# Kernel tuning notes

Hardware: AMD Instinct MI355X
Metric: run time of the kernel (lower is better)

## Reference

```python
import jax, jax.numpy as jnp
import numpy as np

N_NODES = 100000


def _gin_layer(x, edge_index, Wa, ba, Wb, bb):
    # GINConv, eps=0: h_i = MLP(x_i + sum_{j->i} x_j)
    src, dst = edge_index[0], edge_index[1]
    agg = jax.ops.segment_sum(x[src], dst, num_segments=N_NODES)  # [N, d]
    h = x + agg
    h = jax.nn.relu(h @ Wa + ba) @ Wb + bb
    return h


def setup_inputs() -> dict:
    key = jax.random.key(0)
    ks = jax.random.split(key, 8)
    d_in, d_h, E = 128, 128, 1600000
    scale_in = 1.0 / np.sqrt(d_in)
    scale_h = 1.0 / np.sqrt(d_h)
    return {
        "x": jax.random.normal(ks[0], (N_NODES, d_in), dtype=jnp.float32),
        "edge_index": jax.random.randint(ks[1], (2, E), 0, N_NODES, dtype=jnp.int64),
        "batch": jnp.zeros((N_NODES,), dtype=jnp.int64),
        "W1a": jax.random.normal(ks[2], (d_in, d_h), dtype=jnp.float32) * scale_in,
        "b1a": jnp.zeros((d_h,), dtype=jnp.float32),
        "W1b": jax.random.normal(ks[3], (d_h, d_h), dtype=jnp.float32) * scale_h,
        "b1b": jnp.zeros((d_h,), dtype=jnp.float32),
        "W2a": jax.random.normal(ks[4], (d_h, d_h), dtype=jnp.float32) * scale_h,
        "b2a": jnp.zeros((d_h,), dtype=jnp.float32),
        "W2b": jax.random.normal(ks[5], (d_h, d_h), dtype=jnp.float32) * scale_h,
        "b2b": jnp.zeros((d_h,), dtype=jnp.float32),
    }


def reference(x, edge_index, batch, W1a, b1a, W1b, b1b, W2a, b2a, W2b, b2b):
    h = jax.nn.relu(_gin_layer(x, edge_index, W1a, b1a, W1b, b1b))
    h = jax.nn.relu(_gin_layer(h, edge_index, W2a, b2a, W2b, b2b))
    return h
```

## Files before the change

kernel.cpp:

```cpp
#include <hip/hip_runtime.h>
#include <hip/hip_bf16.h>

#define D 128
#define EPB 4096
#define CAP 6144

typedef float f32x4 __attribute__((ext_vector_type(4)));
typedef short short8 __attribute__((ext_vector_type(8)));


__device__ __forceinline__ unsigned bf16_rtn_bits(float x) {
    unsigned u = __float_as_uint(x);
    return (u + 0x7fffu + ((u >> 16) & 1u)) >> 16;
}

__device__ __forceinline__ void addbf8(float* acc, uint4 v) {
    acc[0] += __uint_as_float(v.x << 16);
    acc[1] += __uint_as_float(v.x & 0xffff0000u);
    acc[2] += __uint_as_float(v.y << 16);
    acc[3] += __uint_as_float(v.y & 0xffff0000u);
    acc[4] += __uint_as_float(v.z << 16);
    acc[5] += __uint_as_float(v.z & 0xffff0000u);
    acc[6] += __uint_as_float(v.w << 16);
    acc[7] += __uint_as_float(v.w & 0xffff0000u);
}


__global__ void k_zero(int* __restrict__ p, int n) {
    int i = blockIdx.x * 256 + threadIdx.x;
    if (i < n) p[i] = 0;
}

__global__ __launch_bounds__(256) void k_xtobf(const float4* __restrict__ X, uint4* __restrict__ O, int n8) {
    int i = blockIdx.x * 256 + threadIdx.x;
    if (i >= n8) return;
    float4 a = X[2 * i], b = X[2 * i + 1];
    uint4 o;
    o.x = bf16_rtn_bits(a.x) | (bf16_rtn_bits(a.y) << 16);
    o.y = bf16_rtn_bits(a.z) | (bf16_rtn_bits(a.w) << 16);
    o.z = bf16_rtn_bits(b.x) | (bf16_rtn_bits(b.y) << 16);
    o.w = bf16_rtn_bits(b.z) | (bf16_rtn_bits(b.w) << 16);
    O[i] = o;
}

__global__ void k_wsplit(const float* __restrict__ W, unsigned short* __restrict__ Wt) {
    int i = blockIdx.x * 256 + threadIdx.x;
    int k = i >> 7, n = i & 127;
    Wt[n * 128 + k] = (unsigned short)bf16_rtn_bits(W[i]);
}


__global__ __launch_bounds__(256) void k_bin(const int* __restrict__ src,
                                             const int* __restrict__ dst, int E,
                                             int* __restrict__ gCursor,
                                             unsigned* __restrict__ binned) {
    __shared__ int cnt[512];
    __shared__ int offs[512];
    __shared__ int c2[512];
    __shared__ int gOff[512];
    __shared__ int s[256];
    __shared__ unsigned staged[EPB];
    __shared__ unsigned short bo[EPB];
    int t = threadIdx.x;
    cnt[t] = 0; cnt[t + 256] = 0;
    c2[t] = 0; c2[t + 256] = 0;
    __syncthreads();

    unsigned pk[EPB / 256];
    int bk[EPB / 256];
    int e0 = blockIdx.x * EPB;
#pragma unroll
    for (int i = 0; i < EPB / 256; ++i) {
        int e = e0 + i * 256 + t;
        int b = -1; unsigned p = 0;
        if (e < E) {
            int dv = dst[e], sv = src[e];
            b = dv >> 8;
            p = ((unsigned)sv << 8) | (unsigned)(dv & 255);
            atomicAdd(&cnt[b], 1);
        }
        pk[i] = p; bk[i] = b;
    }
    __syncthreads();
    int v0 = cnt[2 * t], v1 = cnt[2 * t + 1];
    int ps = v0 + v1;
    s[t] = ps;
    __syncthreads();
    for (int off = 1; off < 256; off <<= 1) {
        int tv = (t >= off) ? s[t - off] : 0;
        __syncthreads();
        s[t] += tv;
        __syncthreads();
    }
    int ex = s[t] - ps;
    offs[2 * t] = ex;
    offs[2 * t + 1] = ex + v0;
    if (cnt[2 * t])     gOff[2 * t]     = atomicAdd(&gCursor[2 * t], cnt[2 * t]);
    if (cnt[2 * t + 1]) gOff[2 * t + 1] = atomicAdd(&gCursor[2 * t + 1], cnt[2 * t + 1]);
    __syncthreads();
#pragma unroll
    for (int i = 0; i < EPB / 256; ++i) {
        int b = bk[i];
        if (b >= 0) {
            int p = offs[b] + atomicAdd(&c2[b], 1);
            staged[p] = pk[i];
            bo[p] = (unsigned short)b;
        }
    }
    __syncthreads();
    int total = s[255];
    for (int p = t; p < total; p += 256) {
        int b = bo[p];
        binned[(size_t)b * CAP + gOff[b] + (p - offs[b])] = staged[p];
    }
}

__global__ __launch_bounds__(256) void k_csr(const unsigned* __restrict__ binned,
                                             const int* __restrict__ bucketCnt,
                                             int* __restrict__ alloc,
                                             int2* __restrict__ rowse,
                                             int* __restrict__ colA,
                                             int Nn) {
    __shared__ int hist[256], loc[256], cur[256], s[256];
    __shared__ int baseSh;
    int t = threadIdx.x, b = blockIdx.x;
    int n = bucketCnt[b];
    const unsigned* bp = binned + (size_t)b * CAP;
    hist[t] = 0; cur[t] = 0;
    __syncthreads();
    for (int i = t; i < n; i += 256) atomicAdd(&hist[bp[i] & 255u], 1);
    __syncthreads();
    int v = hist[t];
    s[t] = v;
    __syncthreads();
    for (int off = 1; off < 256; off <<= 1) {
        int tv = (t >= off) ? s[t - off] : 0;
        __syncthreads();
        s[t] += tv;
        __syncthreads();
    }
    loc[t] = s[t] - v;
    if (t == 255) baseSh = atomicAdd(alloc, s[255]);
    __syncthreads();
    int base = baseSh;
    int node = b * 256 + t;
    if (node < Nn) rowse[node] = make_int2(base + loc[t], base + loc[t] + v);
    for (int i = t; i < n; i += 256) {
        unsigned w = bp[i];
        int dl = (int)(w & 255u);
        int p = atomicAdd(&cur[dl], 1);
        colA[base + loc[dl] + p] = (int)(w >> 8);
    }
}


__global__ __launch_bounds__(256) void agg_bf16(const unsigned short* __restrict__ X,
                                                const int2* __restrict__ rowse,
                                                const int* __restrict__ colA,
                                                unsigned short* __restrict__ H, int nnodes) {
    int node = blockIdx.x * 4 + (threadIdx.x >> 6);
    if (node >= nnodes) return;
    int lane = threadIdx.x & 63;
    int qt = lane >> 4, slot = lane & 15;
    const uint4* x4 = (const uint4*)X;
    size_t base = (size_t)node * 16 + slot;

    int2 se = rowse[node];
    int e = se.x, end = se.y;

    float acc[8] = {0.f, 0.f, 0.f, 0.f, 0.f, 0.f, 0.f, 0.f};
    float acc2[8] = {0.f, 0.f, 0.f, 0.f, 0.f, 0.f, 0.f, 0.f};
    if (qt == 0) addbf8(acc, x4[base]);

    for (; e + 16 <= end; e += 16) {
        int s0 = colA[e + qt];
        int s1 = colA[e + 4 + qt];
        int s2 = colA[e + 8 + qt];
        int s3 = colA[e + 12 + qt];
        uint4 v0 = x4[(size_t)s0 * 16 + slot];
        uint4 v1 = x4[(size_t)s1 * 16 + slot];
        uint4 v2 = x4[(size_t)s2 * 16 + slot];
        uint4 v3 = x4[(size_t)s3 * 16 + slot];
        addbf8(acc, v0);
        addbf8(acc2, v1);
        addbf8(acc, v2);
        addbf8(acc2, v3);
    }
    if (e + 8 <= end) {
        int s0 = colA[e + qt];
        int s1 = colA[e + 4 + qt];
        uint4 v0 = x4[(size_t)s0 * 16 + slot];
        uint4 v1 = x4[(size_t)s1 * 16 + slot];
        addbf8(acc, v0);
        addbf8(acc2, v1);
        e += 8;
    }
    for (; e < end; e += 4) {
        int idx = e + qt;
        if (idx < end) {
            int s = colA[idx];
            addbf8(acc, x4[(size_t)s * 16 + slot]);
        }
    }
#pragma unroll
    for (int j = 0; j < 8; ++j) {
        acc[j] += acc2[j];
        acc[j] += __shfl_xor(acc[j], 16);
        acc[j] += __shfl_xor(acc[j], 32);
    }
    if (qt == 0) {
        uint4 o;
        o.x = bf16_rtn_bits(acc[0]) | (bf16_rtn_bits(acc[1]) << 16);
        o.y = bf16_rtn_bits(acc[2]) | (bf16_rtn_bits(acc[3]) << 16);
        o.z = bf16_rtn_bits(acc[4]) | (bf16_rtn_bits(acc[5]) << 16);
        o.w = bf16_rtn_bits(acc[6]) | (bf16_rtn_bits(acc[7]) << 16);
        ((uint4*)H)[base] = o;
    }
}


template <bool OUT_BF16>
__global__ __launch_bounds__(256) void mlp_mfma(const unsigned short* __restrict__ Hb,
                                                const unsigned short* __restrict__ WaT,
                                                const float* __restrict__ ba,
                                                const unsigned short* __restrict__ WbT,
                                                const float* __restrict__ bb,
                                                void* __restrict__ OutP, int nrows) {
    __shared__ unsigned short sh[64 * 128];
    const int tid = threadIdx.x;
    const int rows0 = blockIdx.x * 64;
    const int nvalid = min(64, nrows - rows0);

    const int wv = tid >> 6, l = tid & 63, q = l >> 4, cl = l & 15;

    short8 B1[2][4], B2[2][4];
#pragma unroll
    for (int cf = 0; cf < 2; ++cf) {
        const unsigned short* wa = WaT + (size_t)(wv * 32 + cf * 16 + cl) * 128 + q * 8;
        const unsigned short* wb = WbT + (size_t)(wv * 32 + cf * 16 + cl) * 128 + q * 8;
#pragma unroll
        for (int kk = 0; kk < 4; ++kk) {
            B1[cf][kk] = *(const short8*)(wa + kk * 32);
            B2[cf][kk] = *(const short8*)(wb + kk * 32);
        }
    }

    {
        const uint4* src = (const uint4*)(Hb + (size_t)rows0 * 128);
#pragma unroll
        for (int it = 0; it < 4; ++it) {
            int idx = it * 256 + tid;
            int row = idx >> 4, s16 = idx & 15;
            uint4 v = {0u, 0u, 0u, 0u};
            if (row < nvalid) v = src[idx];
            int byteoff = (row << 8) + ((s16 << 4) ^ ((row & 7) << 4));
            *(uint4*)((char*)sh + byteoff) = v;
        }
    }
    __syncthreads();

    f32x4 acc[4][2];
#pragma unroll
    for (int cf = 0; cf < 2; ++cf) {
        float bv = ba[wv * 32 + cf * 16 + cl];
        f32x4 a = {bv, bv, bv, bv};
#pragma unroll
        for (int m = 0; m < 4; ++m) acc[m][cf] = a;
    }
#pragma unroll
    for (int kk = 0; kk < 4; ++kk) {
        short8 a[4];
#pragma unroll
        for (int m = 0; m < 4; ++m) {
            int row = m * 16 + cl;
            int byteoff = (row << 8) + ((kk * 64 + q * 16) ^ ((row & 7) << 4));
            a[m] = *(const short8*)((const char*)sh + byteoff);
        }
#pragma unroll
        for (int m = 0; m < 4; ++m)
#pragma unroll
            for (int cf = 0; cf < 2; ++cf)
                acc[m][cf] = __builtin_amdgcn_mfma_f32_16x16x32_bf16(a[m], B1[cf][kk], acc[m][cf], 0, 0, 0);
    }
    __syncthreads();

#pragma unroll
    for (int m = 0; m < 4; ++m)
#pragma unroll
        for (int cf = 0; cf < 2; ++cf)
#pragma unroll
            for (int r = 0; r < 4; ++r) {
                int row = m * 16 + q * 4 + r;
                int col = wv * 32 + cf * 16 + cl;
                int byteoff = (row << 8) + ((col * 2) ^ ((row & 7) << 4));
                *(unsigned short*)((char*)sh + byteoff) =
                    (unsigned short)bf16_rtn_bits(fmaxf(acc[m][cf][r], 0.f));
            }
    __syncthreads();

#pragma unroll
    for (int cf = 0; cf < 2; ++cf) {
        float bv = bb[wv * 32 + cf * 16 + cl];
        f32x4 a = {bv, bv, bv, bv};
#pragma unroll
        for (int m = 0; m < 4; ++m) acc[m][cf] = a;
    }
#pragma unroll
    for (int kk = 0; kk < 4; ++kk) {
        short8 a[4];
#pragma unroll
        for (int m = 0; m < 4; ++m) {
            int row = m * 16 + cl;
            int byteoff = (row << 8) + ((kk * 64 + q * 16) ^ ((row & 7) << 4));
            a[m] = *(const short8*)((const char*)sh + byteoff);
        }
#pragma unroll
        for (int m = 0; m < 4; ++m)
#pragma unroll
            for (int cf = 0; cf < 2; ++cf)
                acc[m][cf] = __builtin_amdgcn_mfma_f32_16x16x32_bf16(a[m], B2[cf][kk], acc[m][cf], 0, 0, 0);
    }

#pragma unroll
    for (int m = 0; m < 4; ++m)
#pragma unroll
        for (int cf = 0; cf < 2; ++cf)
#pragma unroll
            for (int r = 0; r < 4; ++r) {
                int row = m * 16 + q * 4 + r;
                if (row < nvalid) {
                    float v = fmaxf(acc[m][cf][r], 0.f);
                    size_t gi = ((size_t)rows0 + row) * 128 + wv * 32 + cf * 16 + cl;
                    if (OUT_BF16)
                        ((unsigned short*)OutP)[gi] = (unsigned short)bf16_rtn_bits(v);
                    else
                        ((float*)OutP)[gi] = v;
                }
            }
}


extern "C" void kernel_launch(void* const* d_in, const int* in_sizes, int n_in,
                              void* d_out, int out_size, void* d_ws, size_t ws_size,
                              hipStream_t stream) {
    const float* x  = (const float*)d_in[0];
    const int*   ei = (const int*)d_in[1];
    const float* W1a = (const float*)d_in[3];
    const float* b1a = (const float*)d_in[4];
    const float* W1b = (const float*)d_in[5];
    const float* b1b = (const float*)d_in[6];
    const float* W2a = (const float*)d_in[7];
    const float* b2a = (const float*)d_in[8];
    const float* W2b = (const float*)d_in[9];
    const float* b2b = (const float*)d_in[10];
    float* out = (float*)d_out;

    const int Nn = in_sizes[0] / D;
    const int E  = in_sizes[1] / 2;
    const int* srcIdx = ei;
    const int* dstIdx = ei + E;
    const int NB = (Nn + 255) >> 8;

    char* w = (char*)d_ws;
    size_t off = 0;
    int2* rowse = (int2*)(w + off);    off += (size_t)Nn * 8;
    off = (off + 255) & ~(size_t)255;
    int* gCursor = (int*)(w + off);    off += (size_t)(NB + 1) * 4;
    int* alloc = gCursor + NB;
    off = (off + 255) & ~(size_t)255;
    int* colA = (int*)(w + off);       off += (size_t)E * 4;
    off = (off + 255) & ~(size_t)255;
    unsigned short* wsp = (unsigned short*)(w + off); off += (size_t)4 * 16384 * 2;
    off = (off + 255) & ~(size_t)255;
    unsigned short* bufA = (unsigned short*)(w + off); off += (size_t)Nn * 128 * 2;
    off = (off + 255) & ~(size_t)255;
    unsigned short* bufB = (unsigned short*)(w + off);
    unsigned* binned = (unsigned*)bufB;

    unsigned short* W1aT = wsp + 0 * 16384;
    unsigned short* W1bT = wsp + 1 * 16384;
    unsigned short* W2aT = wsp + 2 * 16384;
    unsigned short* W2bT = wsp + 3 * 16384;

    const int gBin = (E + EPB - 1) / EPB;

    k_xtobf<<<(Nn * 16 + 255) / 256, 256, 0, stream>>>((const float4*)x, (uint4*)bufA, Nn * 16);
    k_wsplit<<<64, 256, 0, stream>>>(W1a, W1aT);
    k_wsplit<<<64, 256, 0, stream>>>(W1b, W1bT);
    k_wsplit<<<64, 256, 0, stream>>>(W2a, W2aT);
    k_wsplit<<<64, 256, 0, stream>>>(W2b, W2bT);

    k_zero<<<(NB + 1 + 255) / 256, 256, 0, stream>>>(gCursor, NB + 1);
    k_bin<<<gBin, 256, 0, stream>>>(srcIdx, dstIdx, E, gCursor, binned);
    k_csr<<<NB, 256, 0, stream>>>(binned, gCursor, alloc, rowse, colA, Nn);

    const int gAgg = (Nn + 3) / 4;
    const int gMlp = (Nn + 63) / 64;

    agg_bf16<<<gAgg, 256, 0, stream>>>(bufA, rowse, colA, bufB, Nn);
    mlp_mfma<true><<<gMlp, 256, 0, stream>>>(bufB, W1aT, b1a, W1bT, b1b, (void*)bufA, Nn);
    agg_bf16<<<gAgg, 256, 0, stream>>>(bufA, rowse, colA, bufB, Nn);
    mlp_mfma<false><<<gMlp, 256, 0, stream>>>(bufB, W2aT, b2a, W2bT, b2b, (void*)out, Nn);
}
```

Baseline: 241.0 us.

## Fuse neighbor aggregation into MLP kernel via shared-memory staging

Merges the gather-sum aggregation kernel and the two-layer MFMA MLP kernel into one. Each wave aggregates 16 rows directly into the swizzled shared tile, removing the bf16 intermediate write and re-read and two launches per layer. Second-layer weights are now loaded after the first GEMM to cut register pressure. In exchange, the grid shrinks to one block per 64 nodes with sequential per-wave row loops, which lowers memory-level parallelism for the latency-bound gather and may reduce occupancy.

```diff
diff --git a/kernel.cpp b/kernel.cpp
--- a/kernel.cpp
+++ b/kernel.cpp
@@ -154,110 +154,91 @@
 }
 
 
-__global__ __launch_bounds__(256) void agg_bf16(const unsigned short* __restrict__ X,
-                                                const int2* __restrict__ rowse,
-                                                const int* __restrict__ colA,
-                                                unsigned short* __restrict__ H, int nnodes) {
-    int node = blockIdx.x * 4 + (threadIdx.x >> 6);
-    if (node >= nnodes) return;
-    int lane = threadIdx.x & 63;
-    int qt = lane >> 4, slot = lane & 15;
-    const uint4* x4 = (const uint4*)X;
-    size_t base = (size_t)node * 16 + slot;
-
-    int2 se = rowse[node];
-    int e = se.x, end = se.y;
-
-    float acc[8] = {0.f, 0.f, 0.f, 0.f, 0.f, 0.f, 0.f, 0.f};
-    float acc2[8] = {0.f, 0.f, 0.f, 0.f, 0.f, 0.f, 0.f, 0.f};
-    if (qt == 0) addbf8(acc, x4[base]);
-
-    for (; e + 16 <= end; e += 16) {
-        int s0 = colA[e + qt];
-        int s1 = colA[e + 4 + qt];
-        int s2 = colA[e + 8 + qt];
-        int s3 = colA[e + 12 + qt];
-        uint4 v0 = x4[(size_t)s0 * 16 + slot];
-        uint4 v1 = x4[(size_t)s1 * 16 + slot];
-        uint4 v2 = x4[(size_t)s2 * 16 + slot];
-        uint4 v3 = x4[(size_t)s3 * 16 + slot];
-        addbf8(acc, v0);
-        addbf8(acc2, v1);
-        addbf8(acc, v2);
-        addbf8(acc2, v3);
-    }
-    if (e + 8 <= end) {
-        int s0 = colA[e + qt];
-        int s1 = colA[e + 4 + qt];
-        uint4 v0 = x4[(size_t)s0 * 16 + slot];
-        uint4 v1 = x4[(size_t)s1 * 16 + slot];
-        addbf8(acc, v0);
-        addbf8(acc2, v1);
-        e += 8;
-    }
-    for (; e < end; e += 4) {
-        int idx = e + qt;
-        if (idx < end) {
-            int s = colA[idx];
-            addbf8(acc, x4[(size_t)s * 16 + slot]);
-        }
-    }
-#pragma unroll
-    for (int j = 0; j < 8; ++j) {
-        acc[j] += acc2[j];
-        acc[j] += __shfl_xor(acc[j], 16);
-        acc[j] += __shfl_xor(acc[j], 32);
-    }
-    if (qt == 0) {
-        uint4 o;
-        o.x = bf16_rtn_bits(acc[0]) | (bf16_rtn_bits(acc[1]) << 16);
-        o.y = bf16_rtn_bits(acc[2]) | (bf16_rtn_bits(acc[3]) << 16);
-        o.z = bf16_rtn_bits(acc[4]) | (bf16_rtn_bits(acc[5]) << 16);
-        o.w = bf16_rtn_bits(acc[6]) | (bf16_rtn_bits(acc[7]) << 16);
-        ((uint4*)H)[base] = o;
-    }
-}
-
-
 template <bool OUT_BF16>
-__global__ __launch_bounds__(256) void mlp_mfma(const unsigned short* __restrict__ Hb,
-                                                const unsigned short* __restrict__ WaT,
-                                                const float* __restrict__ ba,
-                                                const unsigned short* __restrict__ WbT,
-                                                const float* __restrict__ bb,
-                                                void* __restrict__ OutP, int nrows) {
+__global__ __launch_bounds__(256) void agg_mlp(const unsigned short* __restrict__ Xb,
+                                               const int2* __restrict__ rowse,
+                                               const int* __restrict__ colA,
+                                               const unsigned short* __restrict__ WaT,
+                                               const float* __restrict__ ba,
+                                               const unsigned short* __restrict__ WbT,
+                                               const float* __restrict__ bb,
+                                               void* __restrict__ OutP, int nrows) {
     __shared__ unsigned short sh[64 * 128];
     const int tid = threadIdx.x;
     const int rows0 = blockIdx.x * 64;
     const int nvalid = min(64, nrows - rows0);
 
-    const int wv = tid >> 6, l = tid & 63, q = l >> 4, cl = l & 15;
-
-    short8 B1[2][4], B2[2][4];
+    const int wv = tid >> 6, l = tid & 63, qt = l >> 4, slot = l & 15;
+    const uint4* x4 = (const uint4*)Xb;
+
+    for (int i = 0; i < 16; ++i) {
+        int row = wv * 16 + i;
+        int node = rows0 + row;
+        float acc[8] = {0.f, 0.f, 0.f, 0.f, 0.f, 0.f, 0.f, 0.f};
+        float acc2[8] = {0.f, 0.f, 0.f, 0.f, 0.f, 0.f, 0.f, 0.f};
+        if (node < nrows) {
+            size_t base = (size_t)node * 16 + slot;
+            if (qt == 0) addbf8(acc, x4[base]);
+            int2 se = rowse[node];
+            int e = se.x, end = se.y;
+            for (; e + 16 <= end; e += 16) {
+                int s0 = colA[e + qt];
+                int s1 = colA[e + 4 + qt];
+                int s2 = colA[e + 8 + qt];
+                int s3 = colA[e + 12 + qt];
+                uint4 v0 = x4[(size_t)s0 * 16 + slot];
+                uint4 v1 = x4[(size_t)s1 * 16 + slot];
+                uint4 v2 = x4[(size_t)s2 * 16 + slot];
+                uint4 v3 = x4[(size_t)s3 * 16 + slot];
+                addbf8(acc, v0);
+                addbf8(acc2, v1);
+                addbf8(acc, v2);
+                addbf8(acc2, v3);
+            }
+            if (e + 8 <= end) {
+                int s0 = colA[e + qt];
+                int s1 = colA[e + 4 + qt];
+                uint4 v0 = x4[(size_t)s0 * 16 + slot];
+                uint4 v1 = x4[(size_t)s1 * 16 + slot];
+                addbf8(acc, v0);
+                addbf8(acc2, v1);
+                e += 8;
+            }
+            for (; e < end; e += 4) {
+                int idx = e + qt;
+                if (idx < end) {
+                    int s = colA[idx];
+                    addbf8(acc, x4[(size_t)s * 16 + slot]);
+                }
+            }
+        }
+#pragma unroll
+        for (int j = 0; j < 8; ++j) {
+            acc[j] += acc2[j];
+            acc[j] += __shfl_xor(acc[j], 16);
+            acc[j] += __shfl_xor(acc[j], 32);
+        }
+        if (qt == 0) {
+            uint4 o;
+            o.x = bf16_rtn_bits(acc[0]) | (bf16_rtn_bits(acc[1]) << 16);
+            o.y = bf16_rtn_bits(acc[2]) | (bf16_rtn_bits(acc[3]) << 16);
+            o.z = bf16_rtn_bits(acc[4]) | (bf16_rtn_bits(acc[5]) << 16);
+            o.w = bf16_rtn_bits(acc[6]) | (bf16_rtn_bits(acc[7]) << 16);
+            int byteoff = (row << 8) + ((slot << 4) ^ ((row & 7) << 4));
+            *(uint4*)((char*)sh + byteoff) = o;
+        }
+    }
+    __syncthreads();
+
+    const int q = qt, cl = slot;
+
+    short8 B1[2][4];
 #pragma unroll
     for (int cf = 0; cf < 2; ++cf) {
         const unsigned short* wa = WaT + (size_t)(wv * 32 + cf * 16 + cl) * 128 + q * 8;
-        const unsigned short* wb = WbT + (size_t)(wv * 32 + cf * 16 + cl) * 128 + q * 8;
-#pragma unroll
-        for (int kk = 0; kk < 4; ++kk) {
-            B1[cf][kk] = *(const short8*)(wa + kk * 32);
-            B2[cf][kk] = *(const short8*)(wb + kk * 32);
-        }
-    }
-
-    {
-        const uint4* src = (const uint4*)(Hb + (size_t)rows0 * 128);
-#pragma unroll
-        for (int it = 0; it < 4; ++it) {
-            int idx = it * 256 + tid;
-            int row = idx >> 4, s16 = idx & 15;
-            uint4 v = {0u, 0u, 0u, 0u};
-            if (row < nvalid) v = src[idx];
-            int byteoff = (row << 8) + ((s16 << 4) ^ ((row & 7) << 4));
-            *(uint4*)((char*)sh + byteoff) = v;
-        }
-    }
-    __syncthreads();
+#pragma unroll
+        for (int kk = 0; kk < 4; ++kk) B1[cf][kk] = *(const short8*)(wa + kk * 32);
+    }
 
     f32x4 acc[4][2];
 #pragma unroll
@@ -281,6 +262,14 @@
 #pragma unroll
             for (int cf = 0; cf < 2; ++cf)
                 acc[m][cf] = __builtin_amdgcn_mfma_f32_16x16x32_bf16(a[m], B1[cf][kk], acc[m][cf], 0, 0, 0);
+    }
+
+    short8 B2[2][4];
+#pragma unroll
+    for (int cf = 0; cf < 2; ++cf) {
+        const unsigned short* wb = WbT + (size_t)(wv * 32 + cf * 16 + cl) * 128 + q * 8;
+#pragma unroll
+        for (int kk = 0; kk < 4; ++kk) B2[cf][kk] = *(const short8*)(wb + kk * 32);
     }
     __syncthreads();
 
@@ -394,11 +383,8 @@
     k_bin<<<gBin, 256, 0, stream>>>(srcIdx, dstIdx, E, gCursor, binned);
     k_csr<<<NB, 256, 0, stream>>>(binned, gCursor, alloc, rowse, colA, Nn);
 
-    const int gAgg = (Nn + 3) / 4;
-    const int gMlp = (Nn + 63) / 64;
-
-    agg_bf16<<<gAgg, 256, 0, stream>>>(bufA, rowse, colA, bufB, Nn);
-    mlp_mfma<true><<<gMlp, 256, 0, stream>>>(bufB, W1aT, b1a, W1bT, b1b, (void*)bufA, Nn);
-    agg_bf16<<<gAgg, 256, 0, stream>>>(bufA, rowse, colA, bufB, Nn);
-    mlp_mfma<false><<<gMlp, 256, 0, stream>>>(bufB, W2aT, b2a, W2bT, b2b, (void*)out, Nn);
-}
+    const int gFus = (Nn + 63) / 64;
+
+    agg_mlp<true><<<gFus, 256, 0, stream>>>(bufA, rowse, colA, W1aT, b1a, W1bT, b1b, (void*)bufB, Nn);
+    agg_mlp<false><<<gFus, 256, 0, stream>>>(bufB, rowse, colA, W2aT, b2a, W2bT, b2b, (void*)out, Nn);
+}
```

New measurement: 344.7 us. +43.1%, slower.
